# Kernel tuning notes

Measured on AMD Instinct MI355X. Metric: run time of the kernel, lower is better.

## Reference

```python
import jax, jax.numpy as jnp
import numpy as np

THRESHOLD = 0.005
EPS = 1e-5  # torch instance_norm default eps


def setup_inputs() -> dict:
    key = jax.random.key(0)
    k1, k2, k3 = jax.random.split(key, 3)
    B, C, H, W = 4, 64, 64, 64
    feat = 64
    stdv = 1.0 / np.sqrt(feat)  # matches __init_W_bias__ uniform(-stdv, stdv)
    x = jax.random.normal(k1, (B, C, H, W), dtype=jnp.float32)
    W0 = jax.random.uniform(k2, (1, feat, feat), dtype=jnp.float32, minval=-stdv, maxval=stdv)
    W1 = jax.random.uniform(k3, (1, feat, feat), dtype=jnp.float32, minval=-stdv, maxval=stdv)
    return {"x": x, "W0": W0, "W1": W1}


def _laplacian(xn):
    # xn: [B, N, C] node features (pixels x channels). Built under no_grad in torch.
    norms = jnp.sqrt(jnp.sum(xn * xn, axis=2, keepdims=True))  # [B, N, 1]
    num = jnp.einsum('bnc,bmc->bnm', xn, xn)                    # [B, N, N]
    corr = num / (norms * jnp.swapaxes(norms, 1, 2))
    # relu then threshold -> binary adjacency (threshold > 0, so relu is subsumed)
    A = (corr > THRESHOLD).astype(xn.dtype)
    deg = jnp.sum(A, axis=2)                                    # [B, N]
    d_is = 1.0 / jnp.sqrt(deg)                                  # inverse(sqrt(D)) is diagonal
    return A * d_is[:, :, None] * d_is[:, None, :]              # D^-1/2 A D^-1/2


def _instance_norm(h):
    # torch F.instance_norm on [B, N, F] normalizes over the last dim per (b, n)
    mean = jnp.mean(h, axis=-1, keepdims=True)
    var = jnp.mean((h - mean) ** 2, axis=-1, keepdims=True)
    return (h - mean) / jnp.sqrt(var + EPS)


def reference(x, W0, W1):
    B, C, H, Wd = x.shape
    x_linear = x.reshape(B, C, H * Wd).transpose(0, 2, 1)  # [B, N, C]
    lap = _laplacian(jax.lax.stop_gradient(x_linear))       # adjacency built with no_grad
    for Wk in (W0, W1):
        lx = jnp.einsum('bnm,bmc->bnc', lap, x_linear)      # laplacian diffusion
        h = jnp.einsum('bnc,cf->bnf', lx, Wk[0])            # shared weight (repeat over batch)
        x_linear = jax.nn.relu(_instance_norm(h))
    return x_linear
```

## Files before the change

kernel.cpp:

```cpp
#include <hip/hip_runtime.h>
#include <hip/hip_bf16.h>
#include <cstdint>

#define BB 4
#define CC 64
#define NN 4096
#define NWRD 64
#define TAU 0.005f
#define EPSN 1e-5f

typedef __attribute__((ext_vector_type(8))) short short8;
typedef __attribute__((ext_vector_type(4))) float f32x4;
typedef unsigned long long ull;

__device__ inline unsigned int bf16_rne(float v) {
    unsigned int u = __float_as_uint(v);
    return (u + 0x7FFFu + ((u >> 16) & 1u)) >> 16;
}

__device__ inline void gload_lds16(const void* g, void* lds_base) {
    __builtin_amdgcn_global_load_lds(
        (const __attribute__((address_space(1))) unsigned int*)g,
        (__attribute__((address_space(3))) unsigned int*)lds_base, 16, 0, 0);
}


__global__ __launch_bounds__(256) void k_transpose(const float* __restrict__ x,
                                                   float* __restrict__ xt,
                                                   unsigned short* __restrict__ ynh,
                                                   unsigned short* __restrict__ ynl,
                                                   int* __restrict__ deg) {
    __shared__ float lds[64 * 65];
    int t = threadIdx.x;
    int b = blockIdx.y;
    int n0 = blockIdx.x * 64;
    int gid = (b * (NN / 64) + blockIdx.x) * 256 + t;
    if (gid < BB * NN) deg[gid] = 0;
    #pragma unroll
    for (int i = 0; i < 4; ++i) {
        int c = i * 16 + (t >> 4);
        int nc = (t & 15) * 4;
        float4 v = *(const float4*)(x + ((size_t)(b * CC + c)) * NN + n0 + nc);
        lds[c * 65 + nc + 0] = v.x;
        lds[c * 65 + nc + 1] = v.y;
        lds[c * 65 + nc + 2] = v.z;
        lds[c * 65 + nc + 3] = v.w;
    }
    __syncthreads();
    int l = t & 63, wv = t >> 6;
    for (int i = 0; i < 16; ++i) {
        int n = wv * 16 + i;
        float v = lds[l * 65 + n];
        float s = v * v;
        #pragma unroll
        for (int off = 32; off; off >>= 1) s += __shfl_xor(s, off, 64);
        float yv = v * rsqrtf(s);
        unsigned int hb = bf16_rne(yv);
        float lo = yv - __uint_as_float(hb << 16);
        unsigned int lb = bf16_rne(lo);
        size_t row = (size_t)(b * NN + n0 + n);
        xt[row * CC + l] = v;
        ynh[row * CC + l] = (unsigned short)hb;
        ynl[row * CC + l] = (unsigned short)lb;
    }
}

#define CORR_MC 128
__global__ __launch_bounds__(256) void k_corr(const unsigned short* __restrict__ ynh,
                                              const unsigned short* __restrict__ ynl,
                                              ull* __restrict__ mask,
                                              int* __restrict__ deg) {
    __shared__ unsigned short ldsH[2][CORR_MC * 64];
    __shared__ unsigned short ldsL[2][CORR_MC * 64];
    int t = threadIdx.x;
    int l = t & 63, wv = t >> 6;
    int lc = l & 15, q = l >> 4;
    int b = blockIdx.z;
    int idx = blockIdx.x, I = 0;
    while (idx >= 16 - I) { idx -= 16 - I; ++I; }
    int J = I + idx;
    int n0 = I * 256 + wv * 64;
    int m0 = J * 256;
    const unsigned short* bH = ynh + (size_t)b * NN * CC;
    const unsigned short* bL = ynl + (size_t)b * NN * CC;

    short8 ah[4][2], al[4][2];
    #pragma unroll
    for (int nt = 0; nt < 4; ++nt)
        #pragma unroll
        for (int ks = 0; ks < 2; ++ks) {
            size_t off = (size_t)(n0 + nt * 16 + lc) * CC + (ks * 4 + q) * 8;
            ah[nt][ks] = *(const short8*)(bH + off);
            al[nt][ks] = *(const short8*)(bL + off);
        }

    int rr = l & 15;
    int rsel = rr & 3;
    int qq = rr >> 2;
    int myq = l >> 4;

    auto stage = [&](int mc, int bufi) {
        int mbase = m0 + mc * CORR_MC;
        #pragma unroll
        for (int rd = 0; rd < 4; ++rd) {
            int gu = rd * 256 + wv * 64;
            int g = gu + l;
            int ci = (g & ~7) | ((g & 7) ^ ((g >> 3) & 7));
            gload_lds16(bH + (size_t)mbase * CC + ci * 8, &ldsH[bufi][gu * 8]);
            gload_lds16(bL + (size_t)mbase * CC + ci * 8, &ldsL[bufi][gu * 8]);
        }
    };

    ull wout[4];
    int degacc = 0;
    stage(0, 0);
    for (int mc = 0; mc < 2; ++mc) {
        __syncthreads();
        if (mc == 0) stage(1, 1);
        int bufi = mc & 1;
        ull w0 = 0, w1 = 0;
        #pragma unroll
        for (int tt = 0; tt < 8; ++tt) {
            short8 bh[2], bl[2];
            #pragma unroll
            for (int ks = 0; ks < 2; ++ks) {
                int rowm = tt * 16 + lc;
                int sw = ((ks * 4 + q) ^ (rowm & 7)) * 8;
                bh[ks] = *(const short8*)&ldsH[bufi][rowm * 64 + sw];
                bl[ks] = *(const short8*)&ldsL[bufi][rowm * 64 + sw];
            }
            #pragma unroll
            for (int nt = 0; nt < 4; ++nt) {
                f32x4 acc = {0.f, 0.f, 0.f, 0.f};
                #pragma unroll
                for (int ks = 0; ks < 2; ++ks) {
                    acc = __builtin_amdgcn_mfma_f32_16x16x32_bf16(ah[nt][ks], bh[ks], acc, 0, 0, 0);
                    acc = __builtin_amdgcn_mfma_f32_16x16x32_bf16(ah[nt][ks], bl[ks], acc, 0, 0, 0);
                    acc = __builtin_amdgcn_mfma_f32_16x16x32_bf16(al[nt][ks], bh[ks], acc, 0, 0, 0);
                }
                ull bal[4];
                #pragma unroll
                for (int r = 0; r < 4; ++r)
                    bal[r] = __ballot(acc[r] > TAU);
                ull sa = (rsel & 1) ? bal[1] : bal[0];
                ull sb = (rsel & 1) ? bal[3] : bal[2];
                ull sel = (rsel & 2) ? sb : sa;
                ull part = ((sel >> (qq * 16)) & 0xFFFFull) << ((tt & 3) * 16);
                if (myq == nt) { if (tt < 4) w0 |= part; else w1 |= part; }
            }
        }
        wout[mc * 2 + 0] = w0;
        wout[mc * 2 + 1] = w1;
        degacc += __popcll(w0) + __popcll(w1);
    }

    int row = b * NN + n0 + l;
    #pragma unroll
    for (int c = 0; c < 4; ++c)
        mask[((size_t)(b * NWRD + J * 4 + c)) * NN + n0 + l] = wout[c];
    atomicAdd(&deg[row], degacc);

    if (J > I) {
        __syncthreads();
        ull* sh = (ull*)&ldsH[0][0];
        #pragma unroll
        for (int c = 0; c < 4; ++c) sh[(wv * 64 + l) * 5 + c] = wout[c];
        __syncthreads();
        const ull Mv[6] = {0x00000000FFFFFFFFull, 0x0000FFFF0000FFFFull,
                           0x00FF00FF00FF00FFull, 0x0F0F0F0F0F0F0F0Full,
                           0x3333333333333333ull, 0x5555555555555555ull};
        int dm = 0;
        ull tw[4];
        #pragma unroll
        for (int a = 0; a < 4; ++a) {
            ull xv = sh[(a * 64 + l) * 5 + wv];
            int dd = 32;
            #pragma unroll
            for (int s = 0; s < 6; ++s, dd >>= 1) {
                ull y = __shfl_xor(xv, dd, 64);
                ull M = Mv[s];
                xv = (l & dd) ? ((xv & ~M) | ((y >> dd) & M))
                              : ((xv & M) | ((y << dd) & ~M));
            }
            tw[a] = xv;
            dm += __popcll(xv);
        }
        int mrow = b * NN + J * 256 + wv * 64 + l;
        #pragma unroll
        for (int a = 0; a < 4; ++a)
            mask[((size_t)(b * NWRD + I * 4 + a)) * NN + J * 256 + wv * 64 + l] = tw[a];
        atomicAdd(&deg[mrow], dm);
    }
}

__global__ __launch_bounds__(256) void k_pack(const float* __restrict__ xin,
                                              const int* __restrict__ deg,
                                              unsigned short* __restrict__ yph) {
    __shared__ float lds[32 * 65];
    int t = threadIdx.x;
    int kt = blockIdx.x;
    int b = blockIdx.y;
    size_t ibase = (size_t)b * NN * CC + (size_t)kt * 32 * CC;
    #pragma unroll
    for (int i = 0; i < 2; ++i) {
        int f4 = i * 256 + t;
        int m = f4 >> 4;
        float d = rsqrtf((float)deg[b * NN + kt * 32 + m]);
        float4 v = ((const float4*)(xin + ibase))[f4];
        int c = (f4 & 15) * 4;
        lds[m * 65 + c + 0] = v.x * d;
        lds[m * 65 + c + 1] = v.y * d;
        lds[m * 65 + c + 2] = v.z * d;
        lds[m * 65 + c + 3] = v.w * d;
    }
    __syncthreads();
    size_t obase = (size_t)b * NN * CC + (size_t)kt * 2048;
    int kin = t & 31;
    int chi = t >> 5;
    #pragma unroll
    for (int cg = 0; cg < 8; ++cg) {
        int c = cg * 8 + chi;
        yph[obase + c * 32 + kin] = (unsigned short)bf16_rne(lds[kin * 65 + c]);
    }
}

__global__ __launch_bounds__(512, 2) void k_fused(const ull* __restrict__ mask,
                                                  const unsigned short* __restrict__ yph,
                                                  const int* __restrict__ deg,
                                                  const float* __restrict__ W,
                                                  float* __restrict__ xout,
                                                  unsigned short* __restrict__ xpack) {
    __shared__ __align__(16) float red[8 * 64][68];

    int t = threadIdx.x;
    int l = t & 63, wv = t >> 6;
    int lc = l & 15, q = l >> 4;
    int b = blockIdx.y;
    int n0 = blockIdx.x * 64;
    const unsigned short* src = yph + (size_t)b * NN * CC;

    ull mw[8][4];
    #pragma unroll
    for (int nt = 0; nt < 4; ++nt)
        #pragma unroll
        for (int ch = 0; ch < 8; ++ch)
            mw[ch][nt] = mask[((size_t)(b * NWRD + wv * 8 + ch)) * NN + n0 + nt * 16 + lc];

    f32x4 acc[4][4];
    #pragma unroll
    for (int nt = 0; nt < 4; ++nt)
        #pragma unroll
        for (int tt = 0; tt < 4; ++tt) acc[nt][tt] = f32x4{0.f, 0.f, 0.f, 0.f};

    #pragma unroll
    for (int ch = 0; ch < 8; ++ch) {
        int g0 = wv * 16 + ch * 2;
        #pragma unroll
        for (int kt = 0; kt < 2; ++kt) {
            const unsigned short* bsrc = src + (size_t)(g0 + kt) * 2048;
            short8 bf[4];
            #pragma unroll
            for (int tt = 0; tt < 4; ++tt)
                bf[tt] = *(const short8*)&bsrc[(tt * 16 + lc) * 32 + q * 8];
            union { unsigned int u[4]; short8 v; } a[4];
            #pragma unroll
            for (int nt = 0; nt < 4; ++nt) {
                unsigned int bits = (unsigned int)(mw[ch][nt] >> (kt * 32 + q * 8)) & 0xFFu;
                #pragma unroll
                for (int j = 0; j < 4; ++j)
                    a[nt].u[j] = ((bits >> (2 * j)) & 1u ? 0x3F80u : 0u)
                               | ((bits >> (2 * j + 1)) & 1u ? 0x3F800000u : 0u);
            }
            #pragma unroll
            for (int tt = 0; tt < 4; ++tt)
                #pragma unroll
                for (int nt = 0; nt < 4; ++nt)
                    acc[nt][tt] = __builtin_amdgcn_mfma_f32_16x16x32_bf16(a[nt].v, bf[tt], acc[nt][tt], 0, 0, 0);
        }
    }

    #pragma unroll
    for (int nt = 0; nt < 4; ++nt)
        #pragma unroll
        for (int tt = 0; tt < 4; ++tt)
            #pragma unroll
            for (int r = 0; r < 4; ++r)
                red[wv * 64 + nt * 16 + q * 4 + r][tt * 16 + lc] = acc[nt][tt][r];
    __syncthreads();

    {
        int n = t >> 3, c0 = (t & 7) * 8;
        float dRow = rsqrtf((float)deg[b * NN + n0 + n]);
        float s[8] = {0.f, 0.f, 0.f, 0.f, 0.f, 0.f, 0.f, 0.f};
        #pragma unroll
        for (int w = 0; w < 8; ++w) {
            const float* rp = &red[w * 64 + n][c0];
            #pragma unroll
            for (int j = 0; j < 8; ++j) s[j] += rp[j];
        }
        float* wp = &red[n][c0];
        #pragma unroll
        for (int j = 0; j < 8; ++j) wp[j] = s[j] * dRow;
    }
    __syncthreads();

    float Wreg[64];
    #pragma unroll
    for (int c = 0; c < 64; ++c) Wreg[c] = W[c * 64 + l];
    union { unsigned short s[8]; short8 v; } xv;
    #pragma unroll
    for (int tI = 0; tI < 8; ++tI) {
        int nn = wv * 8 + tI;
        int grow = b * NN + n0 + nn;
        float h = 0.f;
        #pragma unroll
        for (int c4 = 0; c4 < 16; ++c4) {
            float4 s4 = *(const float4*)&red[nn][c4 * 4];
            h += s4.x * Wreg[c4 * 4 + 0] + s4.y * Wreg[c4 * 4 + 1]
               + s4.z * Wreg[c4 * 4 + 2] + s4.w * Wreg[c4 * 4 + 3];
        }
        float mean = h;
        #pragma unroll
        for (int off = 32; off; off >>= 1) mean += __shfl_xor(mean, off, 64);
        mean *= (1.f / 64.f);
        float dv = h - mean;
        float var = dv * dv;
        #pragma unroll
        for (int off = 32; off; off >>= 1) var += __shfl_xor(var, off, 64);
        var *= (1.f / 64.f);
        float o = dv * rsqrtf(var + EPSN);
        o = o > 0.f ? o : 0.f;
        if (xout)
            xout[(size_t)grow * CC + l] = o;
        if (xpack) {
            float dR = rsqrtf((float)deg[grow]);
            xv.s[tI] = (unsigned short)bf16_rne(o * dR);
        }
    }
    if (xpack) {
        size_t base = (size_t)b * NN * CC + (size_t)((n0 >> 5) + (wv >> 2)) * 2048
                    + (size_t)l * 32 + (wv & 3) * 8;
        *(short8*)&xpack[base] = xv.v;
    }
}

extern "C" void kernel_launch(void* const* d_in, const int* in_sizes, int n_in,
                              void* d_out, int out_size, void* d_ws, size_t ws_size,
                              hipStream_t stream) {
    const float* x  = (const float*)d_in[0];
    const float* W0 = (const float*)d_in[1];
    const float* W1 = (const float*)d_in[2];
    float* out = (float*)d_out;

    char* ws = (char*)d_ws;
    ull* mask = (ull*)(ws);
    float* xt = (float*)(ws + ((size_t)8 << 20));
    unsigned short* ynh = (unsigned short*)(ws + ((size_t)12 << 20));
    unsigned short* ynl = (unsigned short*)(ws + ((size_t)14 << 20));
    unsigned short* xp0 = (unsigned short*)(ws + ((size_t)16 << 20));
    unsigned short* xp1 = (unsigned short*)(ws + ((size_t)18 << 20));
    int* deg = (int*)(ws + ((size_t)20 << 20));

    k_transpose<<<dim3(NN / 64, BB), 256, 0, stream>>>(x, xt, ynh, ynl, deg);
    k_corr<<<dim3(136, 1, BB), 256, 0, stream>>>(ynh, ynl, mask, deg);

    k_pack<<<dim3(128, BB), 256, 0, stream>>>(xt, deg, xp0);
    k_fused<<<dim3(NN / 64, BB), 512, 0, stream>>>(mask, xp0, deg, W0, nullptr, xp1);

    k_fused<<<dim3(NN / 64, BB), 512, 0, stream>>>(mask, xp1, deg, W1, out, nullptr);
}
```

Baseline: 140.8 us.

## Merge all stages into one cooperative persistent kernel with grid syncs

Replaces the five separate kernel launches (transpose, correlation, pack, two graph layers) with one cooperative kernel of 256 blocks that runs each stage in turn, separated by grid-wide barriers. The fp32 transposed copy of x is no longer stored; the pack stage rereads x directly and transposes it in shared memory. The goal is to remove launch gaps and intermediate traffic. In exchange the correlation work is spread over fewer, larger blocks, with half-blocks taking two tiles each, and the grid barriers add their own synchronisation cost.

```diff
diff --git a/kernel.cpp b/kernel.cpp
--- a/kernel.cpp
+++ b/kernel.cpp
@@ -1,6 +1,9 @@
 #include <hip/hip_runtime.h>
 #include <hip/hip_bf16.h>
+#include <hip/hip_cooperative_groups.h>
 #include <cstdint>
+
+namespace cg = cooperative_groups;
 
 #define BB 4
 #define CC 64
@@ -8,6 +11,7 @@
 #define NWRD 64
 #define TAU 0.005f
 #define EPSN 1e-5f
+#define CORR_MC 128
 
 typedef __attribute__((ext_vector_type(8))) short short8;
 typedef __attribute__((ext_vector_type(4))) float f32x4;
@@ -25,218 +29,18 @@
 }
 
 
-__global__ __launch_bounds__(256) void k_transpose(const float* __restrict__ x,
-                                                   float* __restrict__ xt,
-                                                   unsigned short* __restrict__ ynh,
-                                                   unsigned short* __restrict__ ynl,
-                                                   int* __restrict__ deg) {
-    __shared__ float lds[64 * 65];
-    int t = threadIdx.x;
-    int b = blockIdx.y;
-    int n0 = blockIdx.x * 64;
-    int gid = (b * (NN / 64) + blockIdx.x) * 256 + t;
-    if (gid < BB * NN) deg[gid] = 0;
-    #pragma unroll
-    for (int i = 0; i < 4; ++i) {
-        int c = i * 16 + (t >> 4);
-        int nc = (t & 15) * 4;
-        float4 v = *(const float4*)(x + ((size_t)(b * CC + c)) * NN + n0 + nc);
-        lds[c * 65 + nc + 0] = v.x;
-        lds[c * 65 + nc + 1] = v.y;
-        lds[c * 65 + nc + 2] = v.z;
-        lds[c * 65 + nc + 3] = v.w;
-    }
-    __syncthreads();
-    int l = t & 63, wv = t >> 6;
-    for (int i = 0; i < 16; ++i) {
-        int n = wv * 16 + i;
-        float v = lds[l * 65 + n];
-        float s = v * v;
-        #pragma unroll
-        for (int off = 32; off; off >>= 1) s += __shfl_xor(s, off, 64);
-        float yv = v * rsqrtf(s);
-        unsigned int hb = bf16_rne(yv);
-        float lo = yv - __uint_as_float(hb << 16);
-        unsigned int lb = bf16_rne(lo);
-        size_t row = (size_t)(b * NN + n0 + n);
-        xt[row * CC + l] = v;
-        ynh[row * CC + l] = (unsigned short)hb;
-        ynl[row * CC + l] = (unsigned short)lb;
-    }
-}
-
-#define CORR_MC 128
-__global__ __launch_bounds__(256) void k_corr(const unsigned short* __restrict__ ynh,
-                                              const unsigned short* __restrict__ ynl,
-                                              ull* __restrict__ mask,
-                                              int* __restrict__ deg) {
-    __shared__ unsigned short ldsH[2][CORR_MC * 64];
-    __shared__ unsigned short ldsL[2][CORR_MC * 64];
-    int t = threadIdx.x;
+__device__ __forceinline__ void fused_layer(const ull* __restrict__ mask,
+                                            const unsigned short* __restrict__ yph,
+                                            const int* __restrict__ deg,
+                                            const float* __restrict__ W,
+                                            float* __restrict__ xout,
+                                            unsigned short* __restrict__ xpack,
+                                            int b, int n0, int t,
+                                            unsigned char* smem) {
+    float (*red)[68] = (float (*)[68])smem;
+
     int l = t & 63, wv = t >> 6;
     int lc = l & 15, q = l >> 4;
-    int b = blockIdx.z;
-    int idx = blockIdx.x, I = 0;
-    while (idx >= 16 - I) { idx -= 16 - I; ++I; }
-    int J = I + idx;
-    int n0 = I * 256 + wv * 64;
-    int m0 = J * 256;
-    const unsigned short* bH = ynh + (size_t)b * NN * CC;
-    const unsigned short* bL = ynl + (size_t)b * NN * CC;
-
-    short8 ah[4][2], al[4][2];
-    #pragma unroll
-    for (int nt = 0; nt < 4; ++nt)
-        #pragma unroll
-        for (int ks = 0; ks < 2; ++ks) {
-            size_t off = (size_t)(n0 + nt * 16 + lc) * CC + (ks * 4 + q) * 8;
-            ah[nt][ks] = *(const short8*)(bH + off);
-            al[nt][ks] = *(const short8*)(bL + off);
-        }
-
-    int rr = l & 15;
-    int rsel = rr & 3;
-    int qq = rr >> 2;
-    int myq = l >> 4;
-
-    auto stage = [&](int mc, int bufi) {
-        int mbase = m0 + mc * CORR_MC;
-        #pragma unroll
-        for (int rd = 0; rd < 4; ++rd) {
-            int gu = rd * 256 + wv * 64;
-            int g = gu + l;
-            int ci = (g & ~7) | ((g & 7) ^ ((g >> 3) & 7));
-            gload_lds16(bH + (size_t)mbase * CC + ci * 8, &ldsH[bufi][gu * 8]);
-            gload_lds16(bL + (size_t)mbase * CC + ci * 8, &ldsL[bufi][gu * 8]);
-        }
-    };
-
-    ull wout[4];
-    int degacc = 0;
-    stage(0, 0);
-    for (int mc = 0; mc < 2; ++mc) {
-        __syncthreads();
-        if (mc == 0) stage(1, 1);
-        int bufi = mc & 1;
-        ull w0 = 0, w1 = 0;
-        #pragma unroll
-        for (int tt = 0; tt < 8; ++tt) {
-            short8 bh[2], bl[2];
-            #pragma unroll
-            for (int ks = 0; ks < 2; ++ks) {
-                int rowm = tt * 16 + lc;
-                int sw = ((ks * 4 + q) ^ (rowm & 7)) * 8;
-                bh[ks] = *(const short8*)&ldsH[bufi][rowm * 64 + sw];
-                bl[ks] = *(const short8*)&ldsL[bufi][rowm * 64 + sw];
-            }
-            #pragma unroll
-            for (int nt = 0; nt < 4; ++nt) {
-                f32x4 acc = {0.f, 0.f, 0.f, 0.f};
-                #pragma unroll
-                for (int ks = 0; ks < 2; ++ks) {
-                    acc = __builtin_amdgcn_mfma_f32_16x16x32_bf16(ah[nt][ks], bh[ks], acc, 0, 0, 0);
-                    acc = __builtin_amdgcn_mfma_f32_16x16x32_bf16(ah[nt][ks], bl[ks], acc, 0, 0, 0);
-                    acc = __builtin_amdgcn_mfma_f32_16x16x32_bf16(al[nt][ks], bh[ks], acc, 0, 0, 0);
-                }
-                ull bal[4];
-                #pragma unroll
-                for (int r = 0; r < 4; ++r)
-                    bal[r] = __ballot(acc[r] > TAU);
-                ull sa = (rsel & 1) ? bal[1] : bal[0];
-                ull sb = (rsel & 1) ? bal[3] : bal[2];
-                ull sel = (rsel & 2) ? sb : sa;
-                ull part = ((sel >> (qq * 16)) & 0xFFFFull) << ((tt & 3) * 16);
-                if (myq == nt) { if (tt < 4) w0 |= part; else w1 |= part; }
-            }
-        }
-        wout[mc * 2 + 0] = w0;
-        wout[mc * 2 + 1] = w1;
-        degacc += __popcll(w0) + __popcll(w1);
-    }
-
-    int row = b * NN + n0 + l;
-    #pragma unroll
-    for (int c = 0; c < 4; ++c)
-        mask[((size_t)(b * NWRD + J * 4 + c)) * NN + n0 + l] = wout[c];
-    atomicAdd(&deg[row], degacc);
-
-    if (J > I) {
-        __syncthreads();
-        ull* sh = (ull*)&ldsH[0][0];
-        #pragma unroll
-        for (int c = 0; c < 4; ++c) sh[(wv * 64 + l) * 5 + c] = wout[c];
-        __syncthreads();
-        const ull Mv[6] = {0x00000000FFFFFFFFull, 0x0000FFFF0000FFFFull,
-                           0x00FF00FF00FF00FFull, 0x0F0F0F0F0F0F0F0Full,
-                           0x3333333333333333ull, 0x5555555555555555ull};
-        int dm = 0;
-        ull tw[4];
-        #pragma unroll
-        for (int a = 0; a < 4; ++a) {
-            ull xv = sh[(a * 64 + l) * 5 + wv];
-            int dd = 32;
-            #pragma unroll
-            for (int s = 0; s < 6; ++s, dd >>= 1) {
-                ull y = __shfl_xor(xv, dd, 64);
-                ull M = Mv[s];
-                xv = (l & dd) ? ((xv & ~M) | ((y >> dd) & M))
-                              : ((xv & M) | ((y << dd) & ~M));
-            }
-            tw[a] = xv;
-            dm += __popcll(xv);
-        }
-        int mrow = b * NN + J * 256 + wv * 64 + l;
-        #pragma unroll
-        for (int a = 0; a < 4; ++a)
-            mask[((size_t)(b * NWRD + I * 4 + a)) * NN + J * 256 + wv * 64 + l] = tw[a];
-        atomicAdd(&deg[mrow], dm);
-    }
-}
-
-__global__ __launch_bounds__(256) void k_pack(const float* __restrict__ xin,
-                                              const int* __restrict__ deg,
-                                              unsigned short* __restrict__ yph) {
-    __shared__ float lds[32 * 65];
-    int t = threadIdx.x;
-    int kt = blockIdx.x;
-    int b = blockIdx.y;
-    size_t ibase = (size_t)b * NN * CC + (size_t)kt * 32 * CC;
-    #pragma unroll
-    for (int i = 0; i < 2; ++i) {
-        int f4 = i * 256 + t;
-        int m = f4 >> 4;
-        float d = rsqrtf((float)deg[b * NN + kt * 32 + m]);
-        float4 v = ((const float4*)(xin + ibase))[f4];
-        int c = (f4 & 15) * 4;
-        lds[m * 65 + c + 0] = v.x * d;
-        lds[m * 65 + c + 1] = v.y * d;
-        lds[m * 65 + c + 2] = v.z * d;
-        lds[m * 65 + c + 3] = v.w * d;
-    }
-    __syncthreads();
-    size_t obase = (size_t)b * NN * CC + (size_t)kt * 2048;
-    int kin = t & 31;
-    int chi = t >> 5;
-    #pragma unroll
-    for (int cg = 0; cg < 8; ++cg) {
-        int c = cg * 8 + chi;
-        yph[obase + c * 32 + kin] = (unsigned short)bf16_rne(lds[kin * 65 + c]);
-    }
-}
-
-__global__ __launch_bounds__(512, 2) void k_fused(const ull* __restrict__ mask,
-                                                  const unsigned short* __restrict__ yph,
-                                                  const int* __restrict__ deg,
-                                                  const float* __restrict__ W,
-                                                  float* __restrict__ xout,
-                                                  unsigned short* __restrict__ xpack) {
-    __shared__ __align__(16) float red[8 * 64][68];
-
-    int t = threadIdx.x;
-    int l = t & 63, wv = t >> 6;
-    int lc = l & 15, q = l >> 4;
-    int b = blockIdx.y;
-    int n0 = blockIdx.x * 64;
     const unsigned short* src = yph + (size_t)b * NN * CC;
 
     ull mw[8][4];
@@ -279,6 +83,7 @@
         }
     }
 
+    __syncthreads();
     #pragma unroll
     for (int nt = 0; nt < 4; ++nt)
         #pragma unroll
@@ -344,6 +149,237 @@
     }
 }
 
+__global__ __launch_bounds__(512, 2) void k_mega(const float* __restrict__ x,
+                                                 const float* __restrict__ W0,
+                                                 const float* __restrict__ W1,
+                                                 float* __restrict__ out,
+                                                 ull* __restrict__ mask,
+                                                 unsigned short* __restrict__ ynh,
+                                                 unsigned short* __restrict__ ynl,
+                                                 unsigned short* __restrict__ xp0,
+                                                 unsigned short* __restrict__ xp1,
+                                                 int* __restrict__ deg) {
+    __shared__ __align__(16) unsigned char smem[512 * 68 * 4];
+    cg::grid_group grid = cg::this_grid();
+    int t = threadIdx.x;
+    int bid = blockIdx.x;
+
+    {
+        float* ltr = (float*)smem;
+        int b = bid >> 6;
+        int n0 = (bid & 63) * 64;
+        int gid = bid * 512 + t;
+        if (gid < BB * NN) deg[gid] = 0;
+        #pragma unroll
+        for (int i = 0; i < 2; ++i) {
+            int idx = i * 512 + t;
+            int c = idx >> 4;
+            int nc = (idx & 15) * 4;
+            float4 v = *(const float4*)(x + ((size_t)(b * CC + c)) * NN + n0 + nc);
+            ltr[c * 65 + nc + 0] = v.x;
+            ltr[c * 65 + nc + 1] = v.y;
+            ltr[c * 65 + nc + 2] = v.z;
+            ltr[c * 65 + nc + 3] = v.w;
+        }
+        __syncthreads();
+        int l = t & 63, wv = t >> 6;
+        #pragma unroll
+        for (int i = 0; i < 8; ++i) {
+            int n = wv * 8 + i;
+            float v = ltr[l * 65 + n];
+            float s = v * v;
+            #pragma unroll
+            for (int off = 32; off; off >>= 1) s += __shfl_xor(s, off, 64);
+            float yv = v * rsqrtf(s);
+            unsigned int hb = bf16_rne(yv);
+            float lo = yv - __uint_as_float(hb << 16);
+            unsigned int lb = bf16_rne(lo);
+            size_t row = (size_t)(b * NN + n0 + n);
+            ynh[row * CC + l] = (unsigned short)hb;
+            ynl[row * CC + l] = (unsigned short)lb;
+        }
+    }
+    grid.sync();
+
+    {
+        int h = t >> 8;
+        int th = t & 255;
+        int l = th & 63, wv = th >> 6;
+        int lc = l & 15, q = l >> 4;
+        unsigned short* ldsH = (unsigned short*)(smem + (size_t)h * 65536);
+        unsigned short* ldsL = ldsH + 16384;
+
+        for (int r = 0; r < 2; ++r) {
+            if (r == 1 && bid >= 16) break;
+            int T = r * 512 + bid * 2 + h;
+            int b = T / 136;
+            int idx = T % 136, I = 0;
+            while (idx >= 16 - I) { idx -= 16 - I; ++I; }
+            int J = I + idx;
+            int n0 = I * 256 + wv * 64;
+            int m0 = J * 256;
+            const unsigned short* bH = ynh + (size_t)b * NN * CC;
+            const unsigned short* bL = ynl + (size_t)b * NN * CC;
+
+            __syncthreads();
+
+            auto stage = [&](int mc, int bufi) {
+                int mbase = m0 + mc * CORR_MC;
+                #pragma unroll
+                for (int rd = 0; rd < 4; ++rd) {
+                    int gu = rd * 256 + wv * 64;
+                    int g = gu + l;
+                    int ci = (g & ~7) | ((g & 7) ^ ((g >> 3) & 7));
+                    gload_lds16(bH + (size_t)mbase * CC + ci * 8, &ldsH[bufi * 8192 + gu * 8]);
+                    gload_lds16(bL + (size_t)mbase * CC + ci * 8, &ldsL[bufi * 8192 + gu * 8]);
+                }
+            };
+            stage(0, 0);
+
+            short8 ah[4][2], al[4][2];
+            #pragma unroll
+            for (int nt = 0; nt < 4; ++nt)
+                #pragma unroll
+                for (int ks = 0; ks < 2; ++ks) {
+                    size_t off = (size_t)(n0 + nt * 16 + lc) * CC + (ks * 4 + q) * 8;
+                    ah[nt][ks] = *(const short8*)(bH + off);
+                    al[nt][ks] = *(const short8*)(bL + off);
+                }
+
+            int rr = l & 15;
+            int rsel = rr & 3;
+            int qq = rr >> 2;
+            int myq = l >> 4;
+
+            ull wout[4];
+            int degacc = 0;
+            for (int mc = 0; mc < 2; ++mc) {
+                __syncthreads();
+                if (mc == 0) stage(1, 1);
+                int bufi = mc & 1;
+                ull w0 = 0, w1 = 0;
+                #pragma unroll
+                for (int tt = 0; tt < 8; ++tt) {
+                    short8 bh[2], bl[2];
+                    #pragma unroll
+                    for (int ks = 0; ks < 2; ++ks) {
+                        int rowm = tt * 16 + lc;
+                        int sw = ((ks * 4 + q) ^ (rowm & 7)) * 8;
+                        bh[ks] = *(const short8*)&ldsH[bufi * 8192 + rowm * 64 + sw];
+                        bl[ks] = *(const short8*)&ldsL[bufi * 8192 + rowm * 64 + sw];
+                    }
+                    #pragma unroll
+                    for (int nt = 0; nt < 4; ++nt) {
+                        f32x4 acc = {0.f, 0.f, 0.f, 0.f};
+                        #pragma unroll
+                        for (int ks = 0; ks < 2; ++ks) {
+                            acc = __builtin_amdgcn_mfma_f32_16x16x32_bf16(ah[nt][ks], bh[ks], acc, 0, 0, 0);
+                            acc = __builtin_amdgcn_mfma_f32_16x16x32_bf16(ah[nt][ks], bl[ks], acc, 0, 0, 0);
+                            acc = __builtin_amdgcn_mfma_f32_16x16x32_bf16(al[nt][ks], bh[ks], acc, 0, 0, 0);
+                        }
+                        ull bal[4];
+                        #pragma unroll
+                        for (int rj = 0; rj < 4; ++rj)
+                            bal[rj] = __ballot(acc[rj] > TAU);
+                        ull sa = (rsel & 1) ? bal[1] : bal[0];
+                        ull sb = (rsel & 1) ? bal[3] : bal[2];
+                        ull sel = (rsel & 2) ? sb : sa;
+                        ull part = ((sel >> (qq * 16)) & 0xFFFFull) << ((tt & 3) * 16);
+                        if (myq == nt) { if (tt < 4) w0 |= part; else w1 |= part; }
+                    }
+                }
+                wout[mc * 2 + 0] = w0;
+                wout[mc * 2 + 1] = w1;
+                degacc += __popcll(w0) + __popcll(w1);
+            }
+
+            int row = b * NN + n0 + l;
+            #pragma unroll
+            for (int c = 0; c < 4; ++c)
+                mask[((size_t)(b * NWRD + J * 4 + c)) * NN + n0 + l] = wout[c];
+            atomicAdd(&deg[row], degacc);
+
+            __syncthreads();
+            ull* sh = (ull*)(smem + (size_t)h * 65536);
+            if (J > I) {
+                #pragma unroll
+                for (int c = 0; c < 4; ++c) sh[(wv * 64 + l) * 5 + c] = wout[c];
+            }
+            __syncthreads();
+            if (J > I) {
+                const ull Mv[6] = {0x00000000FFFFFFFFull, 0x0000FFFF0000FFFFull,
+                                   0x00FF00FF00FF00FFull, 0x0F0F0F0F0F0F0F0Full,
+                                   0x3333333333333333ull, 0x5555555555555555ull};
+                int dm = 0;
+                ull tw[4];
+                #pragma unroll
+                for (int a = 0; a < 4; ++a) {
+                    ull xv = sh[(a * 64 + l) * 5 + wv];
+                    int dd = 32;
+                    #pragma unroll
+                    for (int s = 0; s < 6; ++s, dd >>= 1) {
+                        ull y = __shfl_xor(xv, dd, 64);
+                        ull M = Mv[s];
+                        xv = (l & dd) ? ((xv & ~M) | ((y >> dd) & M))
+                                      : ((xv & M) | ((y << dd) & ~M));
+                    }
+                    tw[a] = xv;
+                    dm += __popcll(xv);
+                }
+                int mrow = b * NN + J * 256 + wv * 64 + l;
+                #pragma unroll
+                for (int a = 0; a < 4; ++a)
+                    mask[((size_t)(b * NWRD + I * 4 + a)) * NN + J * 256 + wv * 64 + l] = tw[a];
+                atomicAdd(&deg[mrow], dm);
+            }
+        }
+    }
+    grid.sync();
+
+    {
+        int h = t >> 8;
+        int th = t & 255;
+        int u = bid * 2 + h;
+        int kt = u & 127, b = u >> 7;
+        float* lp = (float*)smem + (size_t)h * (32 * 65);
+        #pragma unroll
+        for (int i = 0; i < 2; ++i) {
+            int idx = i * 256 + th;
+            int c = idx >> 3;
+            int nq = (idx & 7) * 4;
+            float4 v = *(const float4*)(x + ((size_t)(b * CC + c)) * NN + kt * 32 + nq);
+            lp[(nq + 0) * 65 + c] = v.x;
+            lp[(nq + 1) * 65 + c] = v.y;
+            lp[(nq + 2) * 65 + c] = v.z;
+            lp[(nq + 3) * 65 + c] = v.w;
+        }
+        __syncthreads();
+        size_t obase = (size_t)b * NN * CC + (size_t)kt * 2048;
+        int kin = th & 31;
+        int chi = th >> 5;
+        float d = rsqrtf((float)deg[b * NN + kt * 32 + kin]);
+        #pragma unroll
+        for (int g8 = 0; g8 < 8; ++g8) {
+            int c = g8 * 8 + chi;
+            xp0[obase + c * 32 + kin] = (unsigned short)bf16_rne(lp[kin * 65 + c] * d);
+        }
+    }
+    grid.sync();
+
+    {
+        int b = bid >> 6;
+        int n0 = (bid & 63) * 64;
+        fused_layer(mask, xp0, deg, W0, nullptr, xp1, b, n0, t, smem);
+    }
+    grid.sync();
+
+    {
+        int b = bid >> 6;
+        int n0 = (bid & 63) * 64;
+        fused_layer(mask, xp1, deg, W1, out, nullptr, b, n0, t, smem);
+    }
+}
+
 extern "C" void kernel_launch(void* const* d_in, const int* in_sizes, int n_in,
                               void* d_out, int out_size, void* d_ws, size_t ws_size,
                               hipStream_t stream) {
@@ -354,18 +390,15 @@
 
     char* ws = (char*)d_ws;
     ull* mask = (ull*)(ws);
-    float* xt = (float*)(ws + ((size_t)8 << 20));
-    unsigned short* ynh = (unsigned short*)(ws + ((size_t)12 << 20));
-    unsigned short* ynl = (unsigned short*)(ws + ((size_t)14 << 20));
-    unsigned short* xp0 = (unsigned short*)(ws + ((size_t)16 << 20));
-    unsigned short* xp1 = (unsigned short*)(ws + ((size_t)18 << 20));
-    int* deg = (int*)(ws + ((size_t)20 << 20));
-
-    k_transpose<<<dim3(NN / 64, BB), 256, 0, stream>>>(x, xt, ynh, ynl, deg);
-    k_corr<<<dim3(136, 1, BB), 256, 0, stream>>>(ynh, ynl, mask, deg);
-
-    k_pack<<<dim3(128, BB), 256, 0, stream>>>(xt, deg, xp0);
-    k_fused<<<dim3(NN / 64, BB), 512, 0, stream>>>(mask, xp0, deg, W0, nullptr, xp1);
-
-    k_fused<<<dim3(NN / 64, BB), 512, 0, stream>>>(mask, xp1, deg, W1, out, nullptr);
+    unsigned short* ynh = (unsigned short*)(ws + ((size_t)8 << 20));
+    unsigned short* ynl = (unsigned short*)(ws + ((size_t)10 << 20));
+    unsigned short* xp0 = (unsigned short*)(ws + ((size_t)12 << 20));
+    unsigned short* xp1 = (unsigned short*)(ws + ((size_t)14 << 20));
+    int* deg = (int*)(ws + ((size_t)16 << 20));
+
+    void* args[] = {(void*)&x, (void*)&W0, (void*)&W1, (void*)&out,
+                    (void*)&mask, (void*)&ynh, (void*)&ynl,
+                    (void*)&xp0, (void*)&xp1, (void*)&deg};
+    hipLaunchCooperativeKernel((const void*)k_mega, dim3(256), dim3(512),
+                               args, 0, stream);
 }
```

New measurement: 268.8 us. 90.9% more time.

## Halve fused diffusion row tile and drop fp32 transposed copy of x

Applied to the files above, without the earlier changes.

The fused diffusion+projection kernel now processes 32 rows per block instead of 64. That halves the accumulator and mask registers and doubles the grid, and the launch bound is raised to allow four blocks per CU. Separately, the transpose kernel no longer writes an fp32 transposed copy of x; the pack kernel reads x directly in its original layout and transposes it through LDS. This is meant to improve occupancy and parallelism in the main GEMM-like kernel and save a 4MB write and read, at the cost of re-reading the B operand twice as often per row.

```diff
diff --git a/kernel.cpp b/kernel.cpp
--- a/kernel.cpp
+++ b/kernel.cpp
@@ -26,7 +26,6 @@
 
 
 __global__ __launch_bounds__(256) void k_transpose(const float* __restrict__ x,
-                                                   float* __restrict__ xt,
                                                    unsigned short* __restrict__ ynh,
                                                    unsigned short* __restrict__ ynl,
                                                    int* __restrict__ deg) {
@@ -59,7 +58,6 @@
         float lo = yv - __uint_as_float(hb << 16);
         unsigned int lb = bf16_rne(lo);
         size_t row = (size_t)(b * NN + n0 + n);
-        xt[row * CC + l] = v;
         ynh[row * CC + l] = (unsigned short)hb;
         ynl[row * CC + l] = (unsigned short)lb;
     }
@@ -193,67 +191,63 @@
     }
 }
 
-__global__ __launch_bounds__(256) void k_pack(const float* __restrict__ xin,
+__global__ __launch_bounds__(256) void k_pack(const float* __restrict__ x,
                                               const int* __restrict__ deg,
                                               unsigned short* __restrict__ yph) {
-    __shared__ float lds[32 * 65];
+    __shared__ float lp[32 * 65];
     int t = threadIdx.x;
     int kt = blockIdx.x;
     int b = blockIdx.y;
-    size_t ibase = (size_t)b * NN * CC + (size_t)kt * 32 * CC;
     #pragma unroll
     for (int i = 0; i < 2; ++i) {
-        int f4 = i * 256 + t;
-        int m = f4 >> 4;
-        float d = rsqrtf((float)deg[b * NN + kt * 32 + m]);
-        float4 v = ((const float4*)(xin + ibase))[f4];
-        int c = (f4 & 15) * 4;
-        lds[m * 65 + c + 0] = v.x * d;
-        lds[m * 65 + c + 1] = v.y * d;
-        lds[m * 65 + c + 2] = v.z * d;
-        lds[m * 65 + c + 3] = v.w * d;
+        int idx = i * 256 + t;
+        int c = idx >> 3;
+        int nq = (idx & 7) * 4;
+        float4 v = *(const float4*)(x + ((size_t)(b * CC + c)) * NN + kt * 32 + nq);
+        lp[(nq + 0) * 65 + c] = v.x;
+        lp[(nq + 1) * 65 + c] = v.y;
+        lp[(nq + 2) * 65 + c] = v.z;
+        lp[(nq + 3) * 65 + c] = v.w;
     }
     __syncthreads();
     size_t obase = (size_t)b * NN * CC + (size_t)kt * 2048;
     int kin = t & 31;
     int chi = t >> 5;
-    #pragma unroll
-    for (int cg = 0; cg < 8; ++cg) {
-        int c = cg * 8 + chi;
-        yph[obase + c * 32 + kin] = (unsigned short)bf16_rne(lds[kin * 65 + c]);
-    }
-}
-
-__global__ __launch_bounds__(512, 2) void k_fused(const ull* __restrict__ mask,
+    float d = rsqrtf((float)deg[b * NN + kt * 32 + kin]);
+    #pragma unroll
+    for (int g8 = 0; g8 < 8; ++g8) {
+        int c = g8 * 8 + chi;
+        yph[obase + c * 32 + kin] = (unsigned short)bf16_rne(lp[kin * 65 + c] * d);
+    }
+}
+
+__global__ __launch_bounds__(512, 4) void k_fused(const ull* __restrict__ mask,
                                                   const unsigned short* __restrict__ yph,
                                                   const int* __restrict__ deg,
                                                   const float* __restrict__ W,
                                                   float* __restrict__ xout,
                                                   unsigned short* __restrict__ xpack) {
-    __shared__ __align__(16) float red[8 * 64][68];
+    __shared__ __align__(16) float red[8 * 32][68];
 
     int t = threadIdx.x;
     int l = t & 63, wv = t >> 6;
     int lc = l & 15, q = l >> 4;
     int b = blockIdx.y;
-    int n0 = blockIdx.x * 64;
+    int n0 = blockIdx.x * 32;
     const unsigned short* src = yph + (size_t)b * NN * CC;
 
-    ull mw[8][4];
-    #pragma unroll
-    for (int nt = 0; nt < 4; ++nt)
-        #pragma unroll
-        for (int ch = 0; ch < 8; ++ch)
-            mw[ch][nt] = mask[((size_t)(b * NWRD + wv * 8 + ch)) * NN + n0 + nt * 16 + lc];
-
-    f32x4 acc[4][4];
-    #pragma unroll
-    for (int nt = 0; nt < 4; ++nt)
+    f32x4 acc[2][4];
+    #pragma unroll
+    for (int nt = 0; nt < 2; ++nt)
         #pragma unroll
         for (int tt = 0; tt < 4; ++tt) acc[nt][tt] = f32x4{0.f, 0.f, 0.f, 0.f};
 
     #pragma unroll
     for (int ch = 0; ch < 8; ++ch) {
+        ull mwc[2];
+        #pragma unroll
+        for (int nt = 0; nt < 2; ++nt)
+            mwc[nt] = mask[((size_t)(b * NWRD + wv * 8 + ch)) * NN + n0 + nt * 16 + lc];
         int g0 = wv * 16 + ch * 2;
         #pragma unroll
         for (int kt = 0; kt < 2; ++kt) {
@@ -262,10 +256,10 @@
             #pragma unroll
             for (int tt = 0; tt < 4; ++tt)
                 bf[tt] = *(const short8*)&bsrc[(tt * 16 + lc) * 32 + q * 8];
-            union { unsigned int u[4]; short8 v; } a[4];
-            #pragma unroll
-            for (int nt = 0; nt < 4; ++nt) {
-                unsigned int bits = (unsigned int)(mw[ch][nt] >> (kt * 32 + q * 8)) & 0xFFu;
+            union { unsigned int u[4]; short8 v; } a[2];
+            #pragma unroll
+            for (int nt = 0; nt < 2; ++nt) {
+                unsigned int bits = (unsigned int)(mwc[nt] >> (kt * 32 + q * 8)) & 0xFFu;
                 #pragma unroll
                 for (int j = 0; j < 4; ++j)
                     a[nt].u[j] = ((bits >> (2 * j)) & 1u ? 0x3F80u : 0u)
@@ -274,43 +268,43 @@
             #pragma unroll
             for (int tt = 0; tt < 4; ++tt)
                 #pragma unroll
-                for (int nt = 0; nt < 4; ++nt)
+                for (int nt = 0; nt < 2; ++nt)
                     acc[nt][tt] = __builtin_amdgcn_mfma_f32_16x16x32_bf16(a[nt].v, bf[tt], acc[nt][tt], 0, 0, 0);
         }
     }
 
     #pragma unroll
-    for (int nt = 0; nt < 4; ++nt)
+    for (int nt = 0; nt < 2; ++nt)
         #pragma unroll
         for (int tt = 0; tt < 4; ++tt)
             #pragma unroll
             for (int r = 0; r < 4; ++r)
-                red[wv * 64 + nt * 16 + q * 4 + r][tt * 16 + lc] = acc[nt][tt][r];
+                red[wv * 32 + nt * 16 + q * 4 + r][tt * 16 + lc] = acc[nt][tt][r];
     __syncthreads();
 
     {
-        int n = t >> 3, c0 = (t & 7) * 8;
+        int n = t >> 4, c0 = (t & 15) * 4;
         float dRow = rsqrtf((float)deg[b * NN + n0 + n]);
-        float s[8] = {0.f, 0.f, 0.f, 0.f, 0.f, 0.f, 0.f, 0.f};
+        float s[4] = {0.f, 0.f, 0.f, 0.f};
         #pragma unroll
         for (int w = 0; w < 8; ++w) {
-            const float* rp = &red[w * 64 + n][c0];
-            #pragma unroll
-            for (int j = 0; j < 8; ++j) s[j] += rp[j];
+            const float* rp = &red[w * 32 + n][c0];
+            #pragma unroll
+            for (int j = 0; j < 4; ++j) s[j] += rp[j];
         }
         float* wp = &red[n][c0];
         #pragma unroll
-        for (int j = 0; j < 8; ++j) wp[j] = s[j] * dRow;
+        for (int j = 0; j < 4; ++j) wp[j] = s[j] * dRow;
     }
     __syncthreads();
 
     float Wreg[64];
     #pragma unroll
     for (int c = 0; c < 64; ++c) Wreg[c] = W[c * 64 + l];
-    union { unsigned short s[8]; short8 v; } xv;
-    #pragma unroll
-    for (int tI = 0; tI < 8; ++tI) {
-        int nn = wv * 8 + tI;
+    ull xv = 0;
+    #pragma unroll
+    for (int tI = 0; tI < 4; ++tI) {
+        int nn = wv * 4 + tI;
         int grow = b * NN + n0 + nn;
         float h = 0.f;
         #pragma unroll
@@ -334,13 +328,13 @@
             xout[(size_t)grow * CC + l] = o;
         if (xpack) {
             float dR = rsqrtf((float)deg[grow]);
-            xv.s[tI] = (unsigned short)bf16_rne(o * dR);
+            xv |= (ull)(unsigned short)bf16_rne(o * dR) << (16 * tI);
         }
     }
     if (xpack) {
-        size_t base = (size_t)b * NN * CC + (size_t)((n0 >> 5) + (wv >> 2)) * 2048
-                    + (size_t)l * 32 + (wv & 3) * 8;
-        *(short8*)&xpack[base] = xv.v;
+        size_t base = (size_t)b * NN * CC + (size_t)(n0 >> 5) * 2048
+                    + (size_t)l * 32 + (size_t)wv * 4;
+        *(ull*)&xpack[base] = xv;
     }
 }
 
@@ -354,18 +348,17 @@
 
     char* ws = (char*)d_ws;
     ull* mask = (ull*)(ws);
-    float* xt = (float*)(ws + ((size_t)8 << 20));
-    unsigned short* ynh = (unsigned short*)(ws + ((size_t)12 << 20));
-    unsigned short* ynl = (unsigned short*)(ws + ((size_t)14 << 20));
-    unsigned short* xp0 = (unsigned short*)(ws + ((size_t)16 << 20));
-    unsigned short* xp1 = (unsigned short*)(ws + ((size_t)18 << 20));
-    int* deg = (int*)(ws + ((size_t)20 << 20));
-
-    k_transpose<<<dim3(NN / 64, BB), 256, 0, stream>>>(x, xt, ynh, ynl, deg);
+    unsigned short* ynh = (unsigned short*)(ws + ((size_t)8 << 20));
+    unsigned short* ynl = (unsigned short*)(ws + ((size_t)10 << 20));
+    unsigned short* xp0 = (unsigned short*)(ws + ((size_t)12 << 20));
+    unsigned short* xp1 = (unsigned short*)(ws + ((size_t)14 << 20));
+    int* deg = (int*)(ws + ((size_t)16 << 20));
+
+    k_transpose<<<dim3(NN / 64, BB), 256, 0, stream>>>(x, ynh, ynl, deg);
     k_corr<<<dim3(136, 1, BB), 256, 0, stream>>>(ynh, ynl, mask, deg);
 
-    k_pack<<<dim3(128, BB), 256, 0, stream>>>(xt, deg, xp0);
-    k_fused<<<dim3(NN / 64, BB), 512, 0, stream>>>(mask, xp0, deg, W0, nullptr, xp1);
-
-    k_fused<<<dim3(NN / 64, BB), 512, 0, stream>>>(mask, xp1, deg, W1, out, nullptr);
-}
+    k_pack<<<dim3(128, BB), 256, 0, stream>>>(x, deg, xp0);
+    k_fused<<<dim3(NN / 32, BB), 512, 0, stream>>>(mask, xp0, deg, W0, nullptr, xp1);
+
+    k_fused<<<dim3(NN / 32, BB), 512, 0, stream>>>(mask, xp1, deg, W1, out, nullptr);
+}
```

New measurement: 142.2 us. No clear change (+1.0%).
